# Optimization experiments

Hardware: AMD Instinct MI355X
Metric: run time of the kernel (lower is better)

Reference implementation:

```python
import jax, jax.numpy as jnp
import numpy as np


def setup_inputs() -> dict:
    key = jax.random.key(0)
    k1, k2, k3, k4, k5 = jax.random.split(key, 5)
    B, S, D, H, L = 32, 2048, 512, 32, 2
    inp = jax.random.normal(k1, (B, S, D), dtype=jnp.float32)
    mask = jax.random.randint(k2, (B, S), 0, 2) > 0  # bool [B,S]
    projector = jax.random.normal(k3, (D, H), dtype=jnp.float32) * 0.05
    hidden = jax.random.normal(k4, (L - 1, H, H), dtype=jnp.float32) * 0.05
    evaluator = jax.random.normal(k5, (H, 1), dtype=jnp.float32) * 0.05
    return {"inp": inp, "mask": mask, "projector": projector,
            "hidden": hidden, "evaluator": evaluator}


def reference(inp, mask, projector, hidden, evaluator):
    act = jax.nn.sigmoid
    scale = jnp.asarray(projector.shape[-1], inp.dtype) ** 0.5  # sqrt(hidden_dim)
    m = mask.astype(inp.dtype)[..., None]          # [B,S,1]
    x = inp * m                                     # masked inputs (inp *= mask)
    w = act(jnp.einsum('bsd,dh->bsh', x, projector) / scale)
    for i in range(hidden.shape[0]):                # n_layers - 1 hidden matmuls
        w = act(jnp.einsum('bsh,hk->bsk', w, hidden[i]) / scale)
    w = act(jnp.einsum('bsh,ho->bso', w, evaluator) / scale)  # [B,S,1]
    w = jax.nn.softmax(w, axis=-2)                  # softmax over sequence axis
    w = w * m
    w = w / (jnp.sum(w, axis=1, keepdims=True) + 1e-12)
    return jnp.sum(w * x, axis=1)                   # [B,D]
```

## Files before the change

### kernel.cpp

```cpp
#include <hip/hip_runtime.h>

#define B_   32
#define S_   2048
#define D_   512
#define H_   32
#define BS_  (B_*S_)
#define NTILE_ (BS_/32)
#define TPB_   4
#define GRID_  (NTILE_/TPB_)
#define INV_SCALE 0.17677669529663689f


typedef short  s16x8 __attribute__((ext_vector_type(8)));
typedef float  f32x4 __attribute__((ext_vector_type(4)));

__device__ __forceinline__ float sigmoidf_(float x) {
    return 1.0f / (1.0f + __expf(-x));
}

__device__ __forceinline__ void barrier_lds() {
    asm volatile("s_waitcnt lgkmcnt(0)" ::: "memory");
    __builtin_amdgcn_s_barrier();
    asm volatile("" ::: "memory");
}

#define XST 520
#define WST 36

__global__ __launch_bounds__(256, 2) void kFused(
        const float* __restrict__ inp, const int* __restrict__ mask,
        const float* __restrict__ proj, const float* __restrict__ hd,
        const float* __restrict__ ev,
        float* __restrict__ partial, float2* __restrict__ zdm) {
    __shared__ __align__(16) unsigned short xs[32 * XST];
    __shared__ __align__(16) float w0f[32 * WST];
    __shared__ __align__(16) float hds[32 * 32];
    __shared__ float cs[32];
    __shared__ float es[32];
    __shared__ float mskAll[TPB_ * 32];

    const int tid = threadIdx.x;
    const int wave = tid >> 6, lane = tid & 63;
    const int rt = wave & 1, ct = wave >> 1;
    const int m = lane & 15, quad = lane >> 4;
    const int tile0 = blockIdx.x * TPB_;

    float4 tmp[16];
    {
        const float4* g = (const float4*)inp + (size_t)tile0 * 4096;
        #pragma unroll
        for (int i = 0; i < 16; ++i)
            tmp[i] = g[i * 256 + tid];
    }

    s16x8 bf[16];
    {
        const int col = ct * 16 + m;
        #pragma unroll
        for (int ks = 0; ks < 16; ++ks) {
            float f0 = proj[(size_t)(quad * 8 + ks * 32 + 0) * 32 + col];
            float f1 = proj[(size_t)(quad * 8 + ks * 32 + 1) * 32 + col];
            float f2 = proj[(size_t)(quad * 8 + ks * 32 + 2) * 32 + col];
            float f3 = proj[(size_t)(quad * 8 + ks * 32 + 3) * 32 + col];
            float f4 = proj[(size_t)(quad * 8 + ks * 32 + 4) * 32 + col];
            float f5 = proj[(size_t)(quad * 8 + ks * 32 + 5) * 32 + col];
            float f6 = proj[(size_t)(quad * 8 + ks * 32 + 6) * 32 + col];
            float f7 = proj[(size_t)(quad * 8 + ks * 32 + 7) * 32 + col];
            union { unsigned u[4]; s16x8 v; } bb;
            asm("v_cvt_pk_bf16_f32 %0, %1, %2" : "=v"(bb.u[0]) : "v"(f0), "v"(f1));
            asm("v_cvt_pk_bf16_f32 %0, %1, %2" : "=v"(bb.u[1]) : "v"(f2), "v"(f3));
            asm("v_cvt_pk_bf16_f32 %0, %1, %2" : "=v"(bb.u[2]) : "v"(f4), "v"(f5));
            asm("v_cvt_pk_bf16_f32 %0, %1, %2" : "=v"(bb.u[3]) : "v"(f6), "v"(f7));
            bf[ks] = bb.v;
        }
    }

    const int k = tid & 31, slot = tid >> 5;
    ((float4*)hds)[tid] = ((const float4*)hd)[tid];
    const float evk = ev[k];
    if (tid < TPB_ * 32)
        mskAll[tid] = (mask[tile0 * 32 + tid] != 0) ? 1.0f : 0.0f;

    for (int t = 0; t < TPB_; ++t) {
        const int tile = tile0 + t;
        const float4* g2 = (const float4*)inp + (size_t)(tile + 1) * 4096;
        const bool pf = (t + 1 < TPB_);

        #pragma unroll
        for (int i = 0; i < 16; ++i) {
            int fi = i * 256 + tid;
            int row = fi >> 7, kq = fi & 127;
            unsigned p0, p1;
            asm("v_cvt_pk_bf16_f32 %0, %1, %2" : "=v"(p0) : "v"(tmp[i].x), "v"(tmp[i].y));
            asm("v_cvt_pk_bf16_f32 %0, %1, %2" : "=v"(p1) : "v"(tmp[i].z), "v"(tmp[i].w));
            uint2 u; u.x = p0; u.y = p1;
            *(uint2*)(xs + row * XST + kq * 4) = u;
        }

        if (pf) {
            #pragma unroll
            for (int i = 0; i < 6; ++i)
                tmp[i] = g2[i * 256 + tid];
        }
        barrier_lds();

        const unsigned short* arow = xs + (rt * 16 + m) * XST + quad * 8;
        f32x4 acc = {0.f, 0.f, 0.f, 0.f};
        #pragma unroll
        for (int ks = 0; ks < 16; ++ks) {
            s16x8 a = *(const s16x8*)(arow + ks * 32);
            acc = __builtin_amdgcn_mfma_f32_16x16x32_bf16(a, bf[ks], acc, 0, 0, 0);
        }

        #pragma unroll
        for (int r = 0; r < 4; ++r) {
            int rowL = rt * 16 + quad * 4 + r;
            w0f[rowL * WST + ct * 16 + m] =
                sigmoidf_(mskAll[t * 32 + rowL] * acc[r] * INV_SCALE);
        }
        barrier_lds();

        if (pf) {
            #pragma unroll
            for (int i = 6; i < 11; ++i)
                tmp[i] = g2[i * 256 + tid];
        }

        #pragma unroll
        for (int tt = 0; tt < 4; ++tt) {
            const int row = slot + 8 * tt;
            const float4* wr = (const float4*)(w0f + row * WST);
            float s = 0.f;
            #pragma unroll
            for (int i = 0; i < 8; ++i) {
                float4 w4 = wr[i];
                s = fmaf(w4.x, hds[(4 * i + 0) * 32 + k], s);
                s = fmaf(w4.y, hds[(4 * i + 1) * 32 + k], s);
                s = fmaf(w4.z, hds[(4 * i + 2) * 32 + k], s);
                s = fmaf(w4.w, hds[(4 * i + 3) * 32 + k], s);
            }
            float val = sigmoidf_(s * INV_SCALE) * evk;
            #pragma unroll
            for (int o = 1; o < 32; o <<= 1)
                val += __shfl_xor(val, o);
            if (k == 0) {
                float v2 = sigmoidf_(val * INV_SCALE);
                float e  = __expf(v2);
                es[row] = e;
                cs[row] = mskAll[t * 32 + row] * e;
            }
        }
        barrier_lds();

        if (pf) {
            #pragma unroll
            for (int i = 11; i < 16; ++i)
                tmp[i] = g2[i * 256 + tid];
        }

        if (tid < 64) {
            float z = 0.f, dm = 0.f;
            if (tid < 32) { z = es[tid]; dm = cs[tid]; }
            #pragma unroll
            for (int o = 32; o > 0; o >>= 1) {
                z  += __shfl_down(z, o);
                dm += __shfl_down(dm, o);
            }
            if (tid == 0) zdm[tile] = make_float2(z, dm);
        }

        float a0 = 0.f, a1 = 0.f;
        #pragma unroll 8
        for (int row = 0; row < 32; ++row) {
            unsigned u = *(const unsigned*)(xs + row * XST + 2 * tid);
            float x0 = __uint_as_float(u << 16);
            float x1 = __uint_as_float(u & 0xffff0000u);
            float c = cs[row];
            a0 = fmaf(c, x0, a0);
            a1 = fmaf(c, x1, a1);
        }
        ((float2*)(partial + (size_t)tile * 512))[tid] = make_float2(a0, a1);

        barrier_lds();
    }
}

__global__ __launch_bounds__(1024) void kReduce(
        const float* __restrict__ partial, const float2* __restrict__ zdm,
        float* __restrict__ out) {
    const int b = blockIdx.x, tid = threadIdx.x;
    const int d2 = tid & 255;
    const int g  = tid >> 8;
    __shared__ float sInv;
    __shared__ float2 red[3][256];

    if (tid < 64) {
        float2 p = zdm[b * 64 + tid];
        float z = p.x, dm = p.y;
        #pragma unroll
        for (int o = 32; o > 0; o >>= 1) {
            z  += __shfl_down(z, o);
            dm += __shfl_down(dm, o);
        }
        if (tid == 0) sInv = 1.0f / (dm + 1e-12f * z);
    }

    const float2* pp = (const float2*)partial + (size_t)b * 64 * 256 + d2;
    float2 v[16];
    #pragma unroll
    for (int j = 0; j < 16; ++j)
        v[j] = pp[(size_t)(g * 16 + j) * 256];
    float a = 0.f, c = 0.f;
    #pragma unroll
    for (int j = 0; j < 16; ++j) { a += v[j].x; c += v[j].y; }

    if (g) red[g - 1][d2] = make_float2(a, c);
    __syncthreads();
    if (g == 0) {
        #pragma unroll
        for (int q = 0; q < 3; ++q) { a += red[q][d2].x; c += red[q][d2].y; }
        const float inv = sInv;
        ((float2*)out)[b * 256 + d2] = make_float2(a * inv, c * inv);
    }
}

extern "C" void kernel_launch(void* const* d_in, const int* in_sizes, int n_in,
                              void* d_out, int out_size, void* d_ws, size_t ws_size,
                              hipStream_t stream) {
    const float* inp  = (const float*)d_in[0];
    const int*   mask = (const int*)d_in[1];
    const float* proj = (const float*)d_in[2];
    const float* hid  = (const float*)d_in[3];
    const float* ev   = (const float*)d_in[4];
    float* out = (float*)d_out;

    float2* zdm     = (float2*)((char*)d_ws + 32768);
    float*  partial = (float*)((char*)d_ws + 49152);

    kFused <<<GRID_, 256, 0, stream>>>(inp, mask, proj, hid, ev, partial, zdm);
    kReduce<<<B_, 1024, 0, stream>>>(partial, zdm, out);
}
```

Before: 204.6 us.

## Prefetch two tiles ahead and stage pre-converted bf16 projector in LDS

Adds a small pre-kernel that converts the projector to bf16 in MFMA fragment order. The fused kernel copies it into shared memory and reads B fragments from LDS, instead of holding 16 register vectors of it loaded through strided global reads. The freed registers go to a second 16-float4 staging buffer, so input tiles are prefetched two tiles ahead with alternating buffers. The trade-offs are an extra kernel launch, 32KB more LDS per block, extra LDS reads in the MFMA loop, and register pressure that may hurt the 2-blocks-per-CU occupancy target.

```diff
diff --git a/kernel.cpp b/kernel.cpp
--- a/kernel.cpp
+++ b/kernel.cpp
@@ -18,21 +18,40 @@
     return 1.0f / (1.0f + __expf(-x));
 }
 
+__device__ __forceinline__ unsigned short f2bf(float f) {
+    unsigned u = __float_as_uint(f);
+    u += 0x7fffu + ((u >> 16) & 1u);
+    return (unsigned short)(u >> 16);
+}
+
 __device__ __forceinline__ void barrier_lds() {
     asm volatile("s_waitcnt lgkmcnt(0)" ::: "memory");
     __builtin_amdgcn_s_barrier();
     asm volatile("" ::: "memory");
 }
 
+__global__ void kTransposeBf(const float* __restrict__ P, unsigned short* __restrict__ PTF) {
+    int o = blockIdx.x * 256 + threadIdx.x;
+    int ct = o >> 13;
+    int r1 = o & 8191;
+    int ks = r1 >> 9;
+    int r2 = r1 & 511;
+    int lane = r2 >> 3, e = r2 & 7;
+    int row = (lane >> 4) * 8 + ks * 32 + e;
+    int col = ct * 16 + (lane & 15);
+    PTF[o] = f2bf(P[row * H_ + col]);
+}
+
 #define XST 520
 #define WST 36
 
 __global__ __launch_bounds__(256, 2) void kFused(
         const float* __restrict__ inp, const int* __restrict__ mask,
-        const float* __restrict__ proj, const float* __restrict__ hd,
+        const unsigned short* __restrict__ PTFg, const float* __restrict__ hd,
         const float* __restrict__ ev,
         float* __restrict__ partial, float2* __restrict__ zdm) {
     __shared__ __align__(16) unsigned short xs[32 * XST];
+    __shared__ __align__(16) unsigned short ptf[16384];
     __shared__ __align__(16) float w0f[32 * WST];
     __shared__ __align__(16) float hds[32 * 32];
     __shared__ float cs[32];
@@ -43,56 +62,47 @@
     const int wave = tid >> 6, lane = tid & 63;
     const int rt = wave & 1, ct = wave >> 1;
     const int m = lane & 15, quad = lane >> 4;
+    const int k = tid & 31, slot = tid >> 5;
     const int tile0 = blockIdx.x * TPB_;
 
-    float4 tmp[16];
+    float4 tmpA[16], tmpB[16];
     {
-        const float4* g = (const float4*)inp + (size_t)tile0 * 4096;
+        const float4* g0 = (const float4*)inp + (size_t)tile0 * 4096;
         #pragma unroll
         for (int i = 0; i < 16; ++i)
-            tmp[i] = g[i * 256 + tid];
-    }
-
-    s16x8 bf[16];
+            tmpA[i] = g0[i * 256 + tid];
+        const float4* g1 = g0 + 4096;
+        #pragma unroll
+        for (int i = 0; i < 16; ++i)
+            tmpB[i] = g1[i * 256 + tid];
+    }
+
     {
-        const int col = ct * 16 + m;
-        #pragma unroll
-        for (int ks = 0; ks < 16; ++ks) {
-            float f0 = proj[(size_t)(quad * 8 + ks * 32 + 0) * 32 + col];
-            float f1 = proj[(size_t)(quad * 8 + ks * 32 + 1) * 32 + col];
-            float f2 = proj[(size_t)(quad * 8 + ks * 32 + 2) * 32 + col];
-            float f3 = proj[(size_t)(quad * 8 + ks * 32 + 3) * 32 + col];
-            float f4 = proj[(size_t)(quad * 8 + ks * 32 + 4) * 32 + col];
-            float f5 = proj[(size_t)(quad * 8 + ks * 32 + 5) * 32 + col];
-            float f6 = proj[(size_t)(quad * 8 + ks * 32 + 6) * 32 + col];
-            float f7 = proj[(size_t)(quad * 8 + ks * 32 + 7) * 32 + col];
-            union { unsigned u[4]; s16x8 v; } bb;
-            asm("v_cvt_pk_bf16_f32 %0, %1, %2" : "=v"(bb.u[0]) : "v"(f0), "v"(f1));
-            asm("v_cvt_pk_bf16_f32 %0, %1, %2" : "=v"(bb.u[1]) : "v"(f2), "v"(f3));
-            asm("v_cvt_pk_bf16_f32 %0, %1, %2" : "=v"(bb.u[2]) : "v"(f4), "v"(f5));
-            asm("v_cvt_pk_bf16_f32 %0, %1, %2" : "=v"(bb.u[3]) : "v"(f6), "v"(f7));
-            bf[ks] = bb.v;
-        }
-    }
-
-    const int k = tid & 31, slot = tid >> 5;
+        const uint4* src = (const uint4*)PTFg;
+        uint4* dst = (uint4*)ptf;
+        #pragma unroll
+        for (int i = 0; i < 8; ++i)
+            dst[i * 256 + tid] = src[i * 256 + tid];
+    }
     ((float4*)hds)[tid] = ((const float4*)hd)[tid];
     const float evk = ev[k];
     if (tid < TPB_ * 32)
         mskAll[tid] = (mask[tile0 * 32 + tid] != 0) ? 1.0f : 0.0f;
 
-    for (int t = 0; t < TPB_; ++t) {
+    const unsigned short* bbase = ptf + ct * 8192 + lane * 8;
+
+    auto tileBody = [&](float4 (&tc)[16], const int t) {
         const int tile = tile0 + t;
-        const float4* g2 = (const float4*)inp + (size_t)(tile + 1) * 4096;
-        const bool pf = (t + 1 < TPB_);
+        const bool pf = (t + 2 < TPB_);
+        const float4* g2 = (const float4*)inp + (size_t)(tile + 2) * 4096;
 
         #pragma unroll
         for (int i = 0; i < 16; ++i) {
             int fi = i * 256 + tid;
             int row = fi >> 7, kq = fi & 127;
             unsigned p0, p1;
-            asm("v_cvt_pk_bf16_f32 %0, %1, %2" : "=v"(p0) : "v"(tmp[i].x), "v"(tmp[i].y));
-            asm("v_cvt_pk_bf16_f32 %0, %1, %2" : "=v"(p1) : "v"(tmp[i].z), "v"(tmp[i].w));
+            asm("v_cvt_pk_bf16_f32 %0, %1, %2" : "=v"(p0) : "v"(tc[i].x), "v"(tc[i].y));
+            asm("v_cvt_pk_bf16_f32 %0, %1, %2" : "=v"(p1) : "v"(tc[i].z), "v"(tc[i].w));
             uint2 u; u.x = p0; u.y = p1;
             *(uint2*)(xs + row * XST + kq * 4) = u;
         }
@@ -100,7 +110,7 @@
         if (pf) {
             #pragma unroll
             for (int i = 0; i < 6; ++i)
-                tmp[i] = g2[i * 256 + tid];
+                tc[i] = g2[i * 256 + tid];
         }
         barrier_lds();
 
@@ -109,7 +119,8 @@
         #pragma unroll
         for (int ks = 0; ks < 16; ++ks) {
             s16x8 a = *(const s16x8*)(arow + ks * 32);
-            acc = __builtin_amdgcn_mfma_f32_16x16x32_bf16(a, bf[ks], acc, 0, 0, 0);
+            s16x8 b = *(const s16x8*)(bbase + ks * 512);
+            acc = __builtin_amdgcn_mfma_f32_16x16x32_bf16(a, b, acc, 0, 0, 0);
         }
 
         #pragma unroll
@@ -123,7 +134,7 @@
         if (pf) {
             #pragma unroll
             for (int i = 6; i < 11; ++i)
-                tmp[i] = g2[i * 256 + tid];
+                tc[i] = g2[i * 256 + tid];
         }
 
         #pragma unroll
@@ -155,7 +166,7 @@
         if (pf) {
             #pragma unroll
             for (int i = 11; i < 16; ++i)
-                tmp[i] = g2[i * 256 + tid];
+                tc[i] = g2[i * 256 + tid];
         }
 
         if (tid < 64) {
@@ -182,7 +193,12 @@
         ((float2*)(partial + (size_t)tile * 512))[tid] = make_float2(a0, a1);
 
         barrier_lds();
-    }
+    };
+
+    tileBody(tmpA, 0);
+    tileBody(tmpB, 1);
+    tileBody(tmpA, 2);
+    tileBody(tmpB, 3);
 }
 
 __global__ __launch_bounds__(1024) void kReduce(
@@ -234,9 +250,11 @@
     const float* ev   = (const float*)d_in[4];
     float* out = (float*)d_out;
 
+    unsigned short* PTFg = (unsigned short*)d_ws;
     float2* zdm     = (float2*)((char*)d_ws + 32768);
     float*  partial = (float*)((char*)d_ws + 49152);
 
-    kFused <<<GRID_, 256, 0, stream>>>(inp, mask, proj, hid, ev, partial, zdm);
-    kReduce<<<B_, 1024, 0, stream>>>(partial, zdm, out);
-}
+    kTransposeBf<<<64, 256, 0, stream>>>(proj, PTFg);
+    kFused      <<<GRID_, 256, 0, stream>>>(inp, mask, PTFg, hid, ev, partial, zdm);
+    kReduce     <<<B_, 1024, 0, stream>>>(partial, zdm, out);
+}
```

New measurement: 207.7 us. Within noise of the previous version (+1.5%).

## Fuse final reduction into main kernel via last-block atomic ticket

Applied to the files above, without the earlier changes.

Drops the separate reduction kernel launch. Each block atomically increments a per-batch ticket, and the last of the 16 blocks for a batch reduces that batch's partial sums and normalizer and writes the output. This saves a kernel launch and its gap, but adds a memset launch for the tickets, extra fences, and a serialized tail reduction done by only 256 threads in the last block.

```diff
diff --git a/kernel.cpp b/kernel.cpp
--- a/kernel.cpp
+++ b/kernel.cpp
@@ -31,19 +31,23 @@
         const float* __restrict__ inp, const int* __restrict__ mask,
         const float* __restrict__ proj, const float* __restrict__ hd,
         const float* __restrict__ ev,
-        float* __restrict__ partial, float2* __restrict__ zdm) {
+        float* __restrict__ partial, float2* __restrict__ zdm,
+        int* __restrict__ tickets, float* __restrict__ out) {
     __shared__ __align__(16) unsigned short xs[32 * XST];
     __shared__ __align__(16) float w0f[32 * WST];
     __shared__ __align__(16) float hds[32 * 32];
     __shared__ float cs[32];
     __shared__ float es[32];
     __shared__ float mskAll[TPB_ * 32];
+    __shared__ int   lastFlag;
+    __shared__ float sInvS;
 
     const int tid = threadIdx.x;
     const int wave = tid >> 6, lane = tid & 63;
     const int rt = wave & 1, ct = wave >> 1;
     const int m = lane & 15, quad = lane >> 4;
     const int tile0 = blockIdx.x * TPB_;
+    const int batch = blockIdx.x >> 4;
 
     float4 tmp[16];
     {
@@ -183,45 +187,42 @@
 
         barrier_lds();
     }
-}
-
-__global__ __launch_bounds__(1024) void kReduce(
-        const float* __restrict__ partial, const float2* __restrict__ zdm,
-        float* __restrict__ out) {
-    const int b = blockIdx.x, tid = threadIdx.x;
-    const int d2 = tid & 255;
-    const int g  = tid >> 8;
-    __shared__ float sInv;
-    __shared__ float2 red[3][256];
+
+    __threadfence();
+    __syncthreads();
+    if (tid == 0) {
+        int old = atomicAdd(tickets + batch, 1);
+        lastFlag = (old == 15);
+    }
+    __syncthreads();
+    if (!lastFlag) return;
+    __threadfence();
 
     if (tid < 64) {
-        float2 p = zdm[b * 64 + tid];
+        float2 p = zdm[batch * 64 + tid];
         float z = p.x, dm = p.y;
         #pragma unroll
         for (int o = 32; o > 0; o >>= 1) {
             z  += __shfl_down(z, o);
             dm += __shfl_down(dm, o);
         }
-        if (tid == 0) sInv = 1.0f / (dm + 1e-12f * z);
-    }
-
-    const float2* pp = (const float2*)partial + (size_t)b * 64 * 256 + d2;
-    float2 v[16];
-    #pragma unroll
-    for (int j = 0; j < 16; ++j)
-        v[j] = pp[(size_t)(g * 16 + j) * 256];
+        if (tid == 0) sInvS = 1.0f / (dm + 1e-12f * z);
+    }
+    __syncthreads();
+
+    const float2* pp = (const float2*)partial + (size_t)batch * 64 * 256 + tid;
     float a = 0.f, c = 0.f;
     #pragma unroll
-    for (int j = 0; j < 16; ++j) { a += v[j].x; c += v[j].y; }
-
-    if (g) red[g - 1][d2] = make_float2(a, c);
-    __syncthreads();
-    if (g == 0) {
-        #pragma unroll
-        for (int q = 0; q < 3; ++q) { a += red[q][d2].x; c += red[q][d2].y; }
-        const float inv = sInv;
-        ((float2*)out)[b * 256 + d2] = make_float2(a * inv, c * inv);
-    }
+    for (int jo = 0; jo < 64; jo += 16) {
+        float2 v[16];
+        #pragma unroll
+        for (int j = 0; j < 16; ++j)
+            v[j] = pp[(size_t)(jo + j) * 256];
+        #pragma unroll
+        for (int j = 0; j < 16; ++j) { a += v[j].x; c += v[j].y; }
+    }
+    const float inv = sInvS;
+    ((float2*)out)[batch * 256 + tid] = make_float2(a * inv, c * inv);
 }
 
 extern "C" void kernel_launch(void* const* d_in, const int* in_sizes, int n_in,
@@ -234,9 +235,11 @@
     const float* ev   = (const float*)d_in[4];
     float* out = (float*)d_out;
 
+    int*    tickets = (int*)d_ws;
     float2* zdm     = (float2*)((char*)d_ws + 32768);
     float*  partial = (float*)((char*)d_ws + 49152);
 
-    kFused <<<GRID_, 256, 0, stream>>>(inp, mask, proj, hid, ev, partial, zdm);
-    kReduce<<<B_, 1024, 0, stream>>>(partial, zdm, out);
-}
+    hipMemsetAsync(tickets, 0, 32 * sizeof(int), stream);
+    kFused<<<GRID_, 256, 0, stream>>>(inp, mask, proj, hid, ev,
+                                      partial, zdm, tickets, out);
+}
```

New measurement: 285.9 us. 1.4x slower.
